# Optimization experiments

Measured on AMD Instinct MI355X. Metric: run time of the kernel, lower is better.

## Reference

```python
import jax, jax.numpy as jnp
import numpy as np

N = 10000      # nodes
E = 160000     # edges (before self-loops)
IN = 256       # input feature dim
H = 8          # heads
C1, C2, C3 = 64, 128, 256  # per-head out channels per layer
NEG_SLOPE = 0.2


def setup_inputs() -> dict:
    key = jax.random.key(0)
    ks = jax.random.split(key, 16)
    def glorot(k, shape):
        fan_in = shape[-1]
        return jax.random.normal(k, shape, dtype=jnp.float32) * (1.0 / np.sqrt(fan_in))
    x = jax.random.normal(ks[0], (N, IN), dtype=jnp.float32)
    edge_index = jax.random.randint(ks[1], (2, E), 0, N)
    # layer 1: in=IN, out=64 per head, concat
    W1  = glorot(ks[2], (H * C1, IN))
    as1 = glorot(ks[3], (H, C1)); ad1 = glorot(ks[4], (H, C1))
    b1  = jnp.zeros((H * C1,), jnp.float32)
    # layer 2: in=H*C1, out=128 per head, concat
    W2  = glorot(ks[5], (H * C2, H * C1))
    as2 = glorot(ks[6], (H, C2)); ad2 = glorot(ks[7], (H, C2))
    b2  = jnp.zeros((H * C2,), jnp.float32)
    # layer 3: in=H*C2, out=256 per head, mean over heads
    W3  = glorot(ks[8], (H * C3, H * C2))
    as3 = glorot(ks[9], (H, C3)); ad3 = glorot(ks[10], (H, C3))
    b3  = jnp.zeros((C3,), jnp.float32)
    return {"x": x, "edge_index": edge_index,
            "W1": W1, "as1": as1, "ad1": ad1, "b1": b1,
            "W2": W2, "as2": as2, "ad2": ad2, "b2": b2,
            "W3": W3, "as3": as3, "ad3": ad3, "b3": b3}


def gat_layer(x, src, dst, W, a_src, a_dst, b, concat, num_nodes):
    """PyG-style GATConv (inference, dropout off, self-loops already in src/dst)."""
    heads, c = a_src.shape
    h = (x @ W.T).reshape(num_nodes, heads, c)          # [N,H,C]
    alpha_src = (h * a_src).sum(-1)                      # [N,H]
    alpha_dst = (h * a_dst).sum(-1)                      # [N,H]
    e = jax.nn.leaky_relu(alpha_src[src] + alpha_dst[dst], NEG_SLOPE)  # [E,H]
    # segment softmax over edges grouped by destination node
    m = jax.ops.segment_max(e, dst, num_segments=num_nodes)
    m = jnp.where(jnp.isfinite(m), m, 0.0)
    p = jnp.exp(e - m[dst])                              # [E,H]
    s = jax.ops.segment_sum(p, dst, num_segments=num_nodes)
    alpha = p / (s[dst] + 1e-16)                         # [E,H]
    out = jax.ops.segment_sum(alpha[:, :, None] * h[src], dst,
                              num_segments=num_nodes)    # [N,H,C]
    out = out.reshape(num_nodes, heads * c) if concat else out.mean(axis=1)
    return out + b


def reference(x, edge_index, W1, as1, ad1, b1, W2, as2, ad2, b2, W3, as3, ad3, b3):
    n = x.shape[0]
    loop = jnp.arange(n, dtype=edge_index.dtype)         # add_self_loops=True
    src = jnp.concatenate([edge_index[0], loop])
    dst = jnp.concatenate([edge_index[1], loop])
    h = jax.nn.elu(gat_layer(x, src, dst, W1, as1, ad1, b1, True, n))
    h = jax.nn.elu(gat_layer(h, src, dst, W2, as2, ad2, b2, True, n))
    return gat_layer(h, src, dst, W3, as3, ad3, b3, False, n)
```

## Files before the change

kernel.cpp:

```cpp
#include <hip/hip_runtime.h>
#include <cstdint>

#define NNODES 10000
#define NEDGES 160000
#define TOT_E  (NEDGES + NNODES)
#define HEADS  8
#define MT 625

typedef unsigned short u16;
typedef __attribute__((ext_vector_type(8))) _Float16 h8;
typedef __attribute__((ext_vector_type(4))) _Float16 h4;
typedef __attribute__((ext_vector_type(4))) float f4;

__device__ inline u16 f2h(float x) {
    union { _Float16 h; u16 u; } c; c.h = (_Float16)x; return c.u;
}

__global__ void count_k(const int* __restrict__ ei, int* __restrict__ deg) {
    int i = blockIdx.x * 256 + threadIdx.x;
    if (i >= TOT_E) return;
    int dst = (i < NEDGES) ? ei[NEDGES + i] : (i - NEDGES);
    atomicAdd(deg + dst, 1);
}

__global__ __launch_bounds__(1024) void scan_k(const int* __restrict__ deg,
                                               int* __restrict__ rows) {
    __shared__ int buf[1024];
    int tid = threadIdx.x;
    int base = tid * 10;
    int loc[10]; int s = 0;
    #pragma unroll
    for (int j = 0; j < 10; j++) {
        int i = base + j;
        loc[j] = s;
        s += (i < NNODES) ? deg[i] : 0;
    }
    buf[tid] = s;
    __syncthreads();
    for (int off = 1; off < 1024; off <<= 1) {
        int t = (tid >= off) ? buf[tid - off] : 0;
        __syncthreads();
        buf[tid] += t;
        __syncthreads();
    }
    int ex = tid ? buf[tid - 1] : 0;
    #pragma unroll
    for (int j = 0; j < 10; j++) {
        int i = base + j;
        if (i < NNODES) rows[i] = ex + loc[j];
    }
    if (tid == 1023) rows[NNODES] = buf[1023];
}

__global__ void scatter_k(const int* __restrict__ ei, const int* __restrict__ rows,
                          int* __restrict__ cursor, int* __restrict__ esrc) {
    int i = blockIdx.x * 256 + threadIdx.x;
    if (i >= TOT_E) return;
    int src, dst;
    if (i < NEDGES) { src = ei[i]; dst = ei[NEDGES + i]; }
    else            { src = i - NEDGES; dst = src; }
    int pos = atomicAdd(cursor + dst, 1);
    esrc[rows[dst] + pos] = src;
}

template<int K, int KT>
__device__ inline void cvt_seg(const float* __restrict__ in, u16* __restrict__ out, int t) {
    int lane = t & 63;
    int tmp  = t >> 6;
    int tk   = tmp % KT;
    int tr   = tmp / KT;
    const float* sp = in + (size_t)(tr * 16 + (lane & 15)) * K + tk * 32 + (lane >> 4) * 8;
    float4 v0 = *(const float4*)sp;
    float4 v1 = *(const float4*)(sp + 4);
    ushort4 h0{f2h(v0.x), f2h(v0.y), f2h(v0.z), f2h(v0.w)};
    ushort4 h1{f2h(v1.x), f2h(v1.y), f2h(v1.z), f2h(v1.w)};
    *(ushort4*)(out + (size_t)t * 8)     = h0;
    *(ushort4*)(out + (size_t)t * 8 + 4) = h1;
}

__global__ __launch_bounds__(256) void cvtsw_all(const float* __restrict__ x,
        const float* __restrict__ W1, const float* __restrict__ W2,
        const float* __restrict__ W3, u16* __restrict__ Axs, u16* __restrict__ W1s,
        u16* __restrict__ W2s, u16* __restrict__ W3s) {
    int g = blockIdx.x * 256 + threadIdx.x;
    if (g < 320000)      cvt_seg<256, 8>(x,  Axs, g);
    else if (g < 336384) cvt_seg<256, 8>(W1, W1s, g - 320000);
    else if (g < 401920) cvt_seg<512, 16>(W2, W2s, g - 336384);
    else                 cvt_seg<1024, 32>(W3, W3s, g - 401920);
}

template<int CHEAD>
__global__ __launch_bounds__(64) void gemm_dx(
    const u16* __restrict__ A, const u16* __restrict__ B,
    u16* __restrict__ C16, int N, int K,
    const float* __restrict__ a_s, const float* __restrict__ a_d,
    float* __restrict__ asrc, float* __restrict__ adst)
{
    const int lane = threadIdx.x;
    const int l15 = lane & 15, quad = lane >> 4;
    const int bx = blockIdx.x, by = blockIdx.y;
    const int row0 = by * 128, col0 = bx * 128;
    const int KT = K >> 5;
    const int lo = lane * 8;

    size_t abase[8], bbase[8];
    #pragma unroll
    for (int i = 0; i < 8; i++) {
        int tr = by * 8 + i; if (tr > MT - 1) tr = MT - 1;
        abase[i] = (size_t)tr * KT * 512;
    }
    #pragma unroll
    for (int j = 0; j < 8; j++)
        bbase[j] = (size_t)(bx * 8 + j) * KT * 512;

    f4 acc[8][8];
    #pragma unroll
    for (int i = 0; i < 8; i++)
        #pragma unroll
        for (int j = 0; j < 8; j++)
            acc[i][j] = (f4){0.f, 0.f, 0.f, 0.f};

    h8 a0[8], b0[8], a1[8], b1[8];
    #pragma unroll
    for (int i = 0; i < 8; i++) {
        a0[i] = *(const h8*)(A + abase[i] + lo);
        b0[i] = *(const h8*)(B + bbase[i] + lo);
    }

    for (int t = 0; t < KT; t += 2) {
        const int off1 = (t + 1) * 512 + lo;
        #pragma unroll
        for (int i = 0; i < 8; i++) {
            a1[i] = *(const h8*)(A + abase[i] + off1);
            b1[i] = *(const h8*)(B + bbase[i] + off1);
        }
        #pragma unroll
        for (int j = 0; j < 8; j++)
            #pragma unroll
            for (int i = 0; i < 8; i++)
                acc[i][j] = __builtin_amdgcn_mfma_f32_16x16x32_f16(a0[i], b0[j], acc[i][j], 0, 0, 0);
        if (t + 2 < KT) {
            const int off2 = (t + 2) * 512 + lo;
            #pragma unroll
            for (int i = 0; i < 8; i++) {
                a0[i] = *(const h8*)(A + abase[i] + off2);
                b0[i] = *(const h8*)(B + bbase[i] + off2);
            }
        }
        #pragma unroll
        for (int j = 0; j < 8; j++)
            #pragma unroll
            for (int i = 0; i < 8; i++)
                acc[i][j] = __builtin_amdgcn_mfma_f32_16x16x32_f16(a1[i], b1[j], acc[i][j], 0, 0, 0);
    }

    float av[8], dv[8];
    #pragma unroll
    for (int j = 0; j < 8; j++) {
        av[j] = a_s[col0 + j * 16 + l15];
        dv[j] = a_d[col0 + j * 16 + l15];
    }

    #pragma unroll
    for (int i = 0; i < 8; i++) {
        #pragma unroll
        for (int r = 0; r < 4; r++) {
            int gr = row0 + i * 16 + quad * 4 + r;
            float sA0 = 0.f, sD0 = 0.f, sA1 = 0.f, sD1 = 0.f;
            #pragma unroll
            for (int j = 0; j < 8; j++) {
                float v = acc[i][j][r];
                if (CHEAD == 64 && j >= 4) { sA1 += v * av[j]; sD1 += v * dv[j]; }
                else                       { sA0 += v * av[j]; sD0 += v * dv[j]; }
            }
            #pragma unroll
            for (int m = 1; m < 16; m <<= 1) {
                sA0 += __shfl_xor(sA0, m); sD0 += __shfl_xor(sD0, m);
                if (CHEAD == 64) { sA1 += __shfl_xor(sA1, m); sD1 += __shfl_xor(sD1, m); }
            }
            if (gr < NNODES) {
                u16* cp = C16 + (size_t)gr * N + col0 + l15;
                #pragma unroll
                for (int j = 0; j < 8; j++)
                    cp[j * 16] = f2h(acc[i][j][r]);
                if (l15 == 0) {
                    if (CHEAD == 64) {
                        int hd0 = col0 >> 6;
                        atomicAdd(asrc + gr * HEADS + hd0,     sA0);
                        atomicAdd(adst + gr * HEADS + hd0,     sD0);
                        atomicAdd(asrc + gr * HEADS + hd0 + 1, sA1);
                        atomicAdd(adst + gr * HEADS + hd0 + 1, sD1);
                    } else {
                        int hd = col0 / CHEAD;
                        atomicAdd(asrc + gr * HEADS + hd, sA0);
                        atomicAdd(adst + gr * HEADS + hd, sD0);
                    }
                }
            }
        }
    }
}

template<int C, int MODE>
__global__ __launch_bounds__(512) void agg_k(const u16* __restrict__ h16,
                                             const float* __restrict__ asrc,
                                             const float* __restrict__ adst,
                                             const int* __restrict__ rows,
                                             const int* __restrict__ esrc,
                                             const float* __restrict__ bias,
                                             u16* __restrict__ oh,
                                             float* __restrict__ outf) {
    constexpr int LPE = C / 4;
    constexpr int EPW = 64 / LPE;
    constexpr int U   = (LPE == 64) ? 16 : (LPE == 32) ? 12 : 8;
    __shared__ float red[MODE == 1 ? HEADS * 256 : 8];

    const int n    = blockIdx.x;
    const int hd   = threadIdx.x >> 6;
    const int lane = threadIdx.x & 63;
    const int sub  = lane / LPE;
    const int cl   = lane % LPE;
    const int beg = rows[n], end = rows[n + 1], deg = end - beg;
    const float ad = adst[n * HEADS + hd];

    float4 acc = {0.f, 0.f, 0.f, 0.f};

    auto gather = [&](int e, float pw, int cdeg) {
        for (int j = 0; j < cdeg; j += EPW * U) {
            int   sn[U]; float wg[U];
            #pragma unroll
            for (int u = 0; u < U; u++) {
                int idx = j + sub + EPW * u;
                int   ss = __shfl(e, idx);
                float ww = __shfl(pw, idx);
                bool ok = idx < cdeg;
                sn[u] = ok ? ss : 0;
                wg[u] = ok ? ww : 0.f;
            }
            h4 v[U];
            #pragma unroll
            for (int u = 0; u < U; u++)
                v[u] = *(const h4*)(h16 + (size_t)sn[u] * (HEADS * C) + hd * C + cl * 4);
            #pragma unroll
            for (int u = 0; u < U; u++) {
                acc.x += wg[u] * (float)v[u].x; acc.y += wg[u] * (float)v[u].y;
                acc.z += wg[u] * (float)v[u].z; acc.w += wg[u] * (float)v[u].w;
            }
        }
    };

    if (deg <= 64) {
        int e = 0; float p = 0.f;
        if (lane < deg) {
            e = esrc[beg + lane];
            float lg = asrc[e * HEADS + hd] + ad;
            lg = (lg > 0.f) ? lg : 0.2f * lg;
            p = __expf(lg);
        }
        float s = p;
        #pragma unroll
        for (int off = 32; off; off >>= 1) s += __shfl_xor(s, off);
        float pw = p / (s + 1e-16f);
        gather(e, pw, deg);
    } else {
        float ssum = 0.f;
        for (int i = beg + lane; i < end; i += 64) {
            float lg = asrc[esrc[i] * HEADS + hd] + ad;
            lg = (lg > 0.f) ? lg : 0.2f * lg;
            ssum += __expf(lg);
        }
        #pragma unroll
        for (int off = 32; off; off >>= 1) ssum += __shfl_xor(ssum, off);
        float inv = 1.f / (ssum + 1e-16f);
        for (int c0 = beg; c0 < end; c0 += 64) {
            int cdeg = min(64, end - c0);
            int e = 0; float pw = 0.f;
            if (lane < cdeg) {
                e = esrc[c0 + lane];
                float lg = asrc[e * HEADS + hd] + ad;
                lg = (lg > 0.f) ? lg : 0.2f * lg;
                pw = __expf(lg) * inv;
            }
            gather(e, pw, cdeg);
        }
    }

    #pragma unroll
    for (int m = LPE; m < 64; m <<= 1) {
        acc.x += __shfl_xor(acc.x, m); acc.y += __shfl_xor(acc.y, m);
        acc.z += __shfl_xor(acc.z, m); acc.w += __shfl_xor(acc.w, m);
    }

    if constexpr (MODE == 0) {
        if (sub == 0) {
            const float* bp = bias + hd * C + cl * 4;
            float4 b = *(const float4*)bp;
            float r[4] = {acc.x + b.x, acc.y + b.y, acc.z + b.z, acc.w + b.w};
            #pragma unroll
            for (int j = 0; j < 4; j++)
                r[j] = (r[j] > 0.f) ? r[j] : (expf(r[j]) - 1.f);
            ushort4 hv;
            hv.x = f2h(r[0]); hv.y = f2h(r[1]); hv.z = f2h(r[2]); hv.w = f2h(r[3]);
            constexpr int KTO = (HEADS * C) / 32;
            int c0 = hd * C + cl * 4;
            int tr = n >> 4;
            int tk = c0 >> 5;
            int ln = ((c0 >> 3) & 3) * 16 + (n & 15);
            size_t idx = ((size_t)(tr * KTO + tk) * 64 + ln) * 8 + (c0 & 7);
            *(ushort4*)(oh + idx) = hv;
        }
    } else {
        *(float4*)&red[hd * 256 + lane * 4] = acc;
        __syncthreads();
        int tid = threadIdx.x;
        if (tid < 256) {
            float s = 0.f;
            #pragma unroll
            for (int hh = 0; hh < HEADS; hh++) s += red[hh * 256 + tid];
            outf[(size_t)n * 256 + tid] = s * 0.125f + bias[tid];
        }
    }
}

extern "C" void kernel_launch(void* const* d_in, const int* in_sizes, int n_in,
                              void* d_out, int out_size, void* d_ws, size_t ws_size,
                              hipStream_t stream) {
    const float* x   = (const float*)d_in[0];
    const int*   ei  = (const int*)d_in[1];
    const float* W1  = (const float*)d_in[2];
    const float* as1 = (const float*)d_in[3];
    const float* ad1 = (const float*)d_in[4];
    const float* b1  = (const float*)d_in[5];
    const float* W2  = (const float*)d_in[6];
    const float* as2 = (const float*)d_in[7];
    const float* ad2 = (const float*)d_in[8];
    const float* b2  = (const float*)d_in[9];
    const float* W3  = (const float*)d_in[10];
    const float* as3 = (const float*)d_in[11];
    const float* ad3 = (const float*)d_in[12];
    const float* b3  = (const float*)d_in[13];
    float* out = (float*)d_out;

    int*   deg    = (int*)d_ws;
    int*   cursor = deg + 10240;
    float* az     = (float*)(cursor + 10240);
    float* asrc1 = az,           * adst1 = az + 81920;
    float* asrc2 = az + 163840,  * adst2 = az + 245760;
    float* asrc3 = az + 327680,  * adst3 = az + 409600;
    int*   rows   = (int*)(az + 491520);
    int*   esrc   = rows + 10240;
    u16*   Hh     = (u16*)(esrc + 170240);
    u16*   Af     = Hh + (size_t)NNODES * 2048;
    u16*   Axs    = Af + (size_t)NNODES * 1024;
    u16*   W1s    = Axs + (size_t)NNODES * 256;
    u16*   W2s    = W1s + 512 * 256;
    u16*   W3s    = W2s + 1024 * 512;

    hipMemsetAsync(d_ws, 0, (size_t)(20480 + 491520) * 4, stream);

    count_k<<<(TOT_E + 255) / 256, 256, 0, stream>>>(ei, deg);
    scan_k<<<1, 1024, 0, stream>>>(deg, rows);
    scatter_k<<<(TOT_E + 255) / 256, 256, 0, stream>>>(ei, rows, cursor, esrc);
    cvtsw_all<<<2594, 256, 0, stream>>>(x, W1, W2, W3, Axs, W1s, W2s, W3s);

    gemm_dx<64><<<dim3(4, 79), 64, 0, stream>>>(Axs, W1s, Hh, 512, 256,
                                                as1, ad1, asrc1, adst1);
    agg_k<64, 0><<<NNODES, 512, 0, stream>>>(Hh, asrc1, adst1, rows, esrc, b1, Af, nullptr);

    gemm_dx<128><<<dim3(8, 79), 64, 0, stream>>>(Af, W2s, Hh, 1024, 512,
                                                 as2, ad2, asrc2, adst2);
    agg_k<128, 0><<<NNODES, 512, 0, stream>>>(Hh, asrc2, adst2, rows, esrc, b2, Af, nullptr);

    gemm_dx<256><<<dim3(16, 79), 64, 0, stream>>>(Af, W3s, Hh, 2048, 1024,
                                                  as3, ad3, asrc3, adst3);
    agg_k<256, 1><<<NNODES, 512, 0, stream>>>(Hh, asrc3, adst3, rows, esrc, b3, nullptr, out);
}
```

Measured before the change: 502.5 us.

## Replace register-direct GEMM with LDS-staged triple-buffered 256x128 tile GEMM

The GEMM moves from a single-wave, 128x128 tile kernel that loaded pre-swizzled fragments straight into registers to a 4-wave, 256x128 tile kernel. Tiles are staged in LDS through asynchronous global_load_lds copies, with triple buffering, an XOR swizzle and explicit vmcnt waits. Because of this, the conversion kernel and the aggregation output now use plain row-major fp16 instead of the fragment-swizzled layout. The goal is more reuse per block, better occupancy and overlap of loads with MFMA, at the cost of barriers and LDS pressure.

```diff
diff --git a/kernel.cpp b/kernel.cpp
--- a/kernel.cpp
+++ b/kernel.cpp
@@ -5,15 +5,22 @@
 #define NEDGES 160000
 #define TOT_E  (NEDGES + NNODES)
 #define HEADS  8
-#define MT 625
 
 typedef unsigned short u16;
 typedef __attribute__((ext_vector_type(8))) _Float16 h8;
 typedef __attribute__((ext_vector_type(4))) _Float16 h4;
 typedef __attribute__((ext_vector_type(4))) float f4;
 
+#define WAIT_VM(n) __builtin_amdgcn_s_waitcnt(0x0F70 | (n))
+
 __device__ inline u16 f2h(float x) {
     union { _Float16 h; u16 u; } c; c.h = (_Float16)x; return c.u;
+}
+
+__device__ inline void gld16(const u16* g, u16* l) {
+    __builtin_amdgcn_global_load_lds(
+        (const __attribute__((address_space(1))) void*)g,
+        (__attribute__((address_space(3))) void*)l, 16, 0, 0);
 }
 
 __global__ void count_k(const int* __restrict__ ei, int* __restrict__ deg) {
@@ -63,95 +70,96 @@
     esrc[rows[dst] + pos] = src;
 }
 
-template<int K, int KT>
-__device__ inline void cvt_seg(const float* __restrict__ in, u16* __restrict__ out, int t) {
-    int lane = t & 63;
-    int tmp  = t >> 6;
-    int tk   = tmp % KT;
-    int tr   = tmp / KT;
-    const float* sp = in + (size_t)(tr * 16 + (lane & 15)) * K + tk * 32 + (lane >> 4) * 8;
-    float4 v0 = *(const float4*)sp;
-    float4 v1 = *(const float4*)(sp + 4);
-    ushort4 h0{f2h(v0.x), f2h(v0.y), f2h(v0.z), f2h(v0.w)};
-    ushort4 h1{f2h(v1.x), f2h(v1.y), f2h(v1.z), f2h(v1.w)};
-    *(ushort4*)(out + (size_t)t * 8)     = h0;
-    *(ushort4*)(out + (size_t)t * 8 + 4) = h1;
-}
-
-__global__ __launch_bounds__(256) void cvtsw_all(const float* __restrict__ x,
+__device__ inline void cvt4(const float* __restrict__ in, u16* __restrict__ o, int i) {
+    float4 v = ((const float4*)in)[i];
+    ushort4 h{f2h(v.x), f2h(v.y), f2h(v.z), f2h(v.w)};
+    ((ushort4*)o)[i] = h;
+}
+__global__ __launch_bounds__(256) void cvt_all(const float* __restrict__ x,
         const float* __restrict__ W1, const float* __restrict__ W2,
-        const float* __restrict__ W3, u16* __restrict__ Axs, u16* __restrict__ W1s,
-        u16* __restrict__ W2s, u16* __restrict__ W3s) {
+        const float* __restrict__ W3, u16* __restrict__ xf, u16* __restrict__ W1f,
+        u16* __restrict__ W2f, u16* __restrict__ W3f) {
     int g = blockIdx.x * 256 + threadIdx.x;
-    if (g < 320000)      cvt_seg<256, 8>(x,  Axs, g);
-    else if (g < 336384) cvt_seg<256, 8>(W1, W1s, g - 320000);
-    else if (g < 401920) cvt_seg<512, 16>(W2, W2s, g - 336384);
-    else                 cvt_seg<1024, 32>(W3, W3s, g - 401920);
+    if (g < 640000)       cvt4(x,  xf,  g);
+    else if (g < 672768)  cvt4(W1, W1f, g - 640000);
+    else if (g < 803840)  cvt4(W2, W2f, g - 672768);
+    else if (g < 1328128) cvt4(W3, W3f, g - 803840);
 }
 
 template<int CHEAD>
-__global__ __launch_bounds__(64) void gemm_dx(
+__global__ __launch_bounds__(256, 2) void gemm_f16(
     const u16* __restrict__ A, const u16* __restrict__ B,
-    u16* __restrict__ C16, int N, int K,
+    u16* __restrict__ C16, int M, int N, int K,
     const float* __restrict__ a_s, const float* __restrict__ a_d,
     float* __restrict__ asrc, float* __restrict__ adst)
 {
-    const int lane = threadIdx.x;
+    __shared__ u16 sh[3][12288];
+    const int t = threadIdx.x, lane = t & 63, w = t >> 6;
+    const int row0 = blockIdx.y * 256, col0 = blockIdx.x * 128;
     const int l15 = lane & 15, quad = lane >> 4;
-    const int bx = blockIdx.x, by = blockIdx.y;
-    const int row0 = by * 128, col0 = bx * 128;
-    const int KT = K >> 5;
-    const int lo = lane * 8;
-
-    size_t abase[8], bbase[8];
-    #pragma unroll
-    for (int i = 0; i < 8; i++) {
-        int tr = by * 8 + i; if (tr > MT - 1) tr = MT - 1;
-        abase[i] = (size_t)tr * KT * 512;
-    }
-    #pragma unroll
-    for (int j = 0; j < 8; j++)
-        bbase[j] = (size_t)(bx * 8 + j) * KT * 512;
-
-    f4 acc[8][8];
-    #pragma unroll
-    for (int i = 0; i < 8; i++)
+
+    const int octg = (lane & 3) ^ ((lane >> 3) & 3);
+    const int rl   = lane >> 2;
+    const u16* gp[6]; int lofs[6];
+    #pragma unroll
+    for (int q = 0; q < 6; q++) {
+        int c = w * 6 + q;
+        if (c < 16) {
+            int gr = row0 + c * 16 + rl; if (gr >= M) gr = M - 1;
+            gp[q] = A + (size_t)gr * K + octg * 8;
+            lofs[q] = c * 512;
+        } else {
+            int gc = col0 + (c - 16) * 16 + rl;
+            gp[q] = B + (size_t)gc * K + octg * 8;
+            lofs[q] = 8192 + (c - 16) * 512;
+        }
+    }
+
+    const int sw = (l15 >> 1) & 3;
+    const int po = (quad ^ sw) * 8;
+    const int arow = (w * 64 + l15) * 32;
+    const int brow = 8192 + l15 * 32;
+
+    f4 acc[4][8];
+    #pragma unroll
+    for (int i = 0; i < 4; i++)
         #pragma unroll
         for (int j = 0; j < 8; j++)
             acc[i][j] = (f4){0.f, 0.f, 0.f, 0.f};
 
-    h8 a0[8], b0[8], a1[8], b1[8];
-    #pragma unroll
-    for (int i = 0; i < 8; i++) {
-        a0[i] = *(const h8*)(A + abase[i] + lo);
-        b0[i] = *(const h8*)(B + bbase[i] + lo);
-    }
-
-    for (int t = 0; t < KT; t += 2) {
-        const int off1 = (t + 1) * 512 + lo;
-        #pragma unroll
-        for (int i = 0; i < 8; i++) {
-            a1[i] = *(const h8*)(A + abase[i] + off1);
-            b1[i] = *(const h8*)(B + bbase[i] + off1);
-        }
-        #pragma unroll
-        for (int j = 0; j < 8; j++)
-            #pragma unroll
-            for (int i = 0; i < 8; i++)
-                acc[i][j] = __builtin_amdgcn_mfma_f32_16x16x32_f16(a0[i], b0[j], acc[i][j], 0, 0, 0);
-        if (t + 2 < KT) {
-            const int off2 = (t + 2) * 512 + lo;
-            #pragma unroll
-            for (int i = 0; i < 8; i++) {
-                a0[i] = *(const h8*)(A + abase[i] + off2);
-                b0[i] = *(const h8*)(B + bbase[i] + off2);
-            }
-        }
-        #pragma unroll
-        for (int j = 0; j < 8; j++)
-            #pragma unroll
-            for (int i = 0; i < 8; i++)
-                acc[i][j] = __builtin_amdgcn_mfma_f32_16x16x32_f16(a1[i], b1[j], acc[i][j], 0, 0, 0);
+    const int T = K >> 5;
+
+    #pragma unroll
+    for (int q = 0; q < 6; q++) { gld16(gp[q], &sh[0][lofs[q]]); gp[q] += 32; }
+    #pragma unroll
+    for (int q = 0; q < 6; q++) { gld16(gp[q], &sh[1][lofs[q]]); gp[q] += 32; }
+
+    for (int k = 0; k < T; k++) {
+        if (k + 2 < T) {
+            u16* dst = &sh[(k + 2) % 3][0];
+            #pragma unroll
+            for (int q = 0; q < 6; q++) { gld16(gp[q], dst + lofs[q]); gp[q] += 32; }
+            WAIT_VM(12);
+        } else if (k + 2 == T) {
+            WAIT_VM(6);
+        } else {
+            WAIT_VM(0);
+        }
+        __builtin_amdgcn_s_barrier();
+
+        const u16* sa = &sh[k % 3][0];
+        h8 a[4];
+        #pragma unroll
+        for (int i = 0; i < 4; i++)
+            a[i] = *(const h8*)&sa[arow + i * 512 + po];
+        #pragma unroll
+        for (int j = 0; j < 8; j++) {
+            h8 b = *(const h8*)&sa[brow + j * 512 + po];
+            #pragma unroll
+            for (int i = 0; i < 4; i++)
+                acc[i][j] = __builtin_amdgcn_mfma_f32_16x16x32_f16(a[i], b, acc[i][j], 0, 0, 0);
+        }
+        __builtin_amdgcn_s_barrier();
     }
 
     float av[8], dv[8];
@@ -162,10 +170,10 @@
     }
 
     #pragma unroll
-    for (int i = 0; i < 8; i++) {
+    for (int i = 0; i < 4; i++) {
         #pragma unroll
         for (int r = 0; r < 4; r++) {
-            int gr = row0 + i * 16 + quad * 4 + r;
+            int gr = row0 + w * 64 + i * 16 + quad * 4 + r;
             float sA0 = 0.f, sD0 = 0.f, sA1 = 0.f, sD1 = 0.f;
             #pragma unroll
             for (int j = 0; j < 8; j++) {
@@ -178,7 +186,7 @@
                 sA0 += __shfl_xor(sA0, m); sD0 += __shfl_xor(sD0, m);
                 if (CHEAD == 64) { sA1 += __shfl_xor(sA1, m); sD1 += __shfl_xor(sD1, m); }
             }
-            if (gr < NNODES) {
+            if (gr < M) {
                 u16* cp = C16 + (size_t)gr * N + col0 + l15;
                 #pragma unroll
                 for (int j = 0; j < 8; j++)
@@ -301,13 +309,7 @@
                 r[j] = (r[j] > 0.f) ? r[j] : (expf(r[j]) - 1.f);
             ushort4 hv;
             hv.x = f2h(r[0]); hv.y = f2h(r[1]); hv.z = f2h(r[2]); hv.w = f2h(r[3]);
-            constexpr int KTO = (HEADS * C) / 32;
-            int c0 = hd * C + cl * 4;
-            int tr = n >> 4;
-            int tk = c0 >> 5;
-            int ln = ((c0 >> 3) & 3) * 16 + (n & 15);
-            size_t idx = ((size_t)(tr * KTO + tk) * 64 + ln) * 8 + (c0 & 7);
-            *(ushort4*)(oh + idx) = hv;
+            *(ushort4*)(oh + (size_t)n * (HEADS * C) + hd * C + cl * 4) = hv;
         }
     } else {
         *(float4*)&red[hd * 256 + lane * 4] = acc;
@@ -351,27 +353,29 @@
     int*   esrc   = rows + 10240;
     u16*   Hh     = (u16*)(esrc + 170240);
     u16*   Af     = Hh + (size_t)NNODES * 2048;
-    u16*   Axs    = Af + (size_t)NNODES * 1024;
-    u16*   W1s    = Axs + (size_t)NNODES * 256;
-    u16*   W2s    = W1s + 512 * 256;
-    u16*   W3s    = W2s + 1024 * 512;
+    u16*   Axf    = Af + (size_t)NNODES * 1024;
+    u16*   W1f    = Axf + (size_t)NNODES * 256;
+    u16*   W2f    = W1f + 512 * 256;
+    u16*   W3f    = W2f + 1024 * 512;
 
     hipMemsetAsync(d_ws, 0, (size_t)(20480 + 491520) * 4, stream);
 
     count_k<<<(TOT_E + 255) / 256, 256, 0, stream>>>(ei, deg);
     scan_k<<<1, 1024, 0, stream>>>(deg, rows);
     scatter_k<<<(TOT_E + 255) / 256, 256, 0, stream>>>(ei, rows, cursor, esrc);
-    cvtsw_all<<<2594, 256, 0, stream>>>(x, W1, W2, W3, Axs, W1s, W2s, W3s);
-
-    gemm_dx<64><<<dim3(4, 79), 64, 0, stream>>>(Axs, W1s, Hh, 512, 256,
-                                                as1, ad1, asrc1, adst1);
+    cvt_all<<<(1328128 + 255) / 256, 256, 0, stream>>>(x, W1, W2, W3, Axf, W1f, W2f, W3f);
+
+    const int rb = (NNODES + 255) / 256;
+
+    gemm_f16<64><<<dim3(4, rb), 256, 0, stream>>>(Axf, W1f, Hh, NNODES, 512, 256,
+                                                  as1, ad1, asrc1, adst1);
     agg_k<64, 0><<<NNODES, 512, 0, stream>>>(Hh, asrc1, adst1, rows, esrc, b1, Af, nullptr);
 
-    gemm_dx<128><<<dim3(8, 79), 64, 0, stream>>>(Af, W2s, Hh, 1024, 512,
-                                                 as2, ad2, asrc2, adst2);
+    gemm_f16<128><<<dim3(8, rb), 256, 0, stream>>>(Af, W2f, Hh, NNODES, 1024, 512,
+                                                   as2, ad2, asrc2, adst2);
     agg_k<128, 0><<<NNODES, 512, 0, stream>>>(Hh, asrc2, adst2, rows, esrc, b2, Af, nullptr);
 
-    gemm_dx<256><<<dim3(16, 79), 64, 0, stream>>>(Af, W3s, Hh, 2048, 1024,
-                                                  as3, ad3, asrc3, adst3);
+    gemm_f16<256><<<dim3(16, rb), 256, 0, stream>>>(Af, W3f, Hh, NNODES, 2048, 1024,
+                                                    as3, ad3, asrc3, adst3);
     agg_k<256, 1><<<NNODES, 512, 0, stream>>>(Hh, asrc3, adst3, rows, esrc, b3, nullptr, out);
 }
```

Measured after the change: 438.9 us. -12.7%, faster.
